# Performance work log

Measured on AMD Instinct MI355X. Metric: run time of the kernel, lower is better.

## Reference

```python
import jax, jax.numpy as jnp
import numpy as np

D = 16        # attention features
H = 8         # heads (head_dim = 2)
L = 8         # encoder layers
FF = 16       # dim_feedforward
K = 35        # conv kernel = stride
SEQ_IN = 3500 # input length -> 100 patches
EPS = 1e-5


def layer_norm(x, g, b):
    mu = jnp.mean(x, axis=-1, keepdims=True)
    var = jnp.mean((x - mu) ** 2, axis=-1, keepdims=True)
    return (x - mu) * jax.lax.rsqrt(var + EPS) * g + b


def setup_inputs() -> dict:
    key = jax.random.key(0)
    ks = jax.random.split(key, 24)
    B = 2048
    s = 0.1
    inp = {
        "x": jax.random.normal(ks[0], (B, SEQ_IN), dtype=jnp.float32),
        "conv_w": jax.random.normal(ks[1], (D, K), dtype=jnp.float32) * s,   # Conv1d(1->16,k=35)
        "conv_b": jax.random.normal(ks[2], (D,), dtype=jnp.float32) * s,
        "cls_emb": jax.random.normal(ks[3], (1, 1, D), dtype=jnp.float32),
        # stacked per-layer params [L, ...]
        "Wqkv": jax.random.normal(ks[4], (L, 3 * D, D), dtype=jnp.float32) * s,
        "bqkv": jnp.zeros((L, 3 * D), dtype=jnp.float32),
        "Wo": jax.random.normal(ks[5], (L, D, D), dtype=jnp.float32) * s,
        "bo": jnp.zeros((L, D), dtype=jnp.float32),
        "W1": jax.random.normal(ks[6], (L, FF, D), dtype=jnp.float32) * s,
        "b1": jnp.zeros((L, FF), dtype=jnp.float32),
        "W2": jax.random.normal(ks[7], (L, D, FF), dtype=jnp.float32) * s,
        "b2": jnp.zeros((L, D), dtype=jnp.float32),
        "ln1_g": jnp.ones((L, D), dtype=jnp.float32),
        "ln1_b": jnp.zeros((L, D), dtype=jnp.float32),
        "ln2_g": jnp.ones((L, D), dtype=jnp.float32),
        "ln2_b": jnp.zeros((L, D), dtype=jnp.float32),
        "lnf_g": jnp.ones((D,), dtype=jnp.float32),
        "lnf_b": jnp.zeros((D,), dtype=jnp.float32),
        "end_w": jax.random.normal(ks[8], (100, D), dtype=jnp.float32) * s,  # Conv1d(16->100,k=1)
        "end_b": jnp.zeros((100,), dtype=jnp.float32),
        "head_w": jax.random.normal(ks[9], (1, 100), dtype=jnp.float32) * s, # Linear(100->1)
        "head_b": jnp.zeros((1,), dtype=jnp.float32),
    }
    return inp


def _forward(x, conv_w, conv_b, cls_emb, Wqkv, bqkv, Wo, bo, W1, b1, W2, b2,
             ln1_g, ln1_b, ln2_g, ln2_b, lnf_g, lnf_b, end_w, end_b, head_w, head_b):
    B = x.shape[0]
    # patch embed: stride==kernel Conv1d == blocked matmul. [B,100,35] @ [35,16]
    patches = x.reshape(B, SEQ_IN // K, K)
    h = jnp.einsum("bpk,fk->bpf", patches, conv_w) + conv_b  # [B,100,16]
    h = jnp.concatenate([jnp.broadcast_to(cls_emb, (B, 1, D)), h], axis=1)  # [B,101,16]
    S = h.shape[1]
    scale = 1.0 / jnp.sqrt(jnp.asarray(D // H, dtype=h.dtype))

    def layer(hc, p):
        wqkv, bq, wo, bob, w1, b1l, w2, b2l, g1, be1, g2, be2 = p
        qkv = jnp.einsum("bsd,ed->bse", hc, wqkv) + bq      # [B,S,48]
        q, k, v = jnp.split(qkv, 3, axis=-1)
        q = q.reshape(B, S, H, D // H)
        k = k.reshape(B, S, H, D // H)
        v = v.reshape(B, S, H, D // H)
        scores = jnp.einsum("bshd,bthd->bhst", q, k) * scale  # [B,H,S,S]
        attn = jax.nn.softmax(scores, axis=-1)
        ctx = jnp.einsum("bhst,bthd->bshd", attn, v).reshape(B, S, D)
        attn_out = jnp.einsum("bsd,od->bso", ctx, wo) + bob
        hc = layer_norm(hc + attn_out, g1, be1)               # post-norm
        ff = jnp.einsum("bsd,fd->bsf", hc, w1) + b1l
        ff = jnp.einsum("bsf,df->bsd", jax.nn.relu(ff), w2) + b2l
        hc = layer_norm(hc + ff, g2, be2)
        return hc, None

    params = (Wqkv, bqkv, Wo, bo, W1, b1, W2, b2, ln1_g, ln1_b, ln2_g, ln2_b)
    h, _ = jax.lax.scan(layer, h, params)
    h = layer_norm(h, lnf_g, lnf_b)
    cls = h[:, 0, :]                                          # [B,16]
    latent = cls @ end_w.T + end_b                            # 1x1 conv == linear, [B,100]
    logits = latent @ head_w.T + head_b                       # [B,1]
    return jax.nn.sigmoid(logits)


def reference(x, conv_w, conv_b, cls_emb, Wqkv, bqkv, Wo, bo, W1, b1, W2, b2,
              ln1_g, ln1_b, ln2_g, ln2_b, lnf_g, lnf_b, end_w, end_b, head_w, head_b):
    return _forward(x, conv_w, conv_b, cls_emb, Wqkv, bqkv, Wo, bo, W1, b1, W2, b2,
                    ln1_g, ln1_b, ln2_g, ln2_b, lnf_g, lnf_b, end_w, end_b, head_w, head_b)
```

## Files before the change

kernel.cpp:

```cpp
#include <hip/hip_runtime.h>
#include <math.h>

#define DD   16
#define NH   8
#define NL   8
#define FFD  16
#define KK   35
#define SEQ  3500
#define NP   100
#define SS   101
#define NBATCH 2
#define NT   256
#define ROWDW 20
#define NROW 102
#define NWPAIR 6144

typedef __fp16 h2 __attribute__((ext_vector_type(2)));

__device__ __forceinline__ float fdot2(h2 a, h2 b, float c) {
#if __has_builtin(__builtin_amdgcn_fdot2)
  return __builtin_amdgcn_fdot2(a, b, c, false);
#else
  return c + (float)a.x * (float)b.x + (float)a.y * (float)b.y;
#endif
}
__device__ __forceinline__ float exp2_fast(float x) {
#if __has_builtin(__builtin_amdgcn_exp2f)
  return __builtin_amdgcn_exp2f(x);
#else
  return exp2f(x);
#endif
}
__device__ __forceinline__ float rcp_fast(float x) {
#if __has_builtin(__builtin_amdgcn_rcpf)
  return __builtin_amdgcn_rcpf(x);
#else
  return 1.0f / x;
#endif
}
__device__ __forceinline__ h2 pk_h2(float a, float b) {
#if __has_builtin(__builtin_amdgcn_cvt_pkrtz)
  return __builtin_amdgcn_cvt_pkrtz(a, b);
#else
  h2 r; r.x = (__fp16)a; r.y = (__fp16)b; return r;
#endif
}
__device__ __forceinline__ unsigned pk_u(float a, float b) {
  return __builtin_bit_cast(unsigned, pk_h2(a, b));
}
__device__ __forceinline__ h2 as_h2(unsigned u) {
  return __builtin_bit_cast(h2, u);
}

__device__ __forceinline__ void lnorm16(float* h, const float* __restrict__ g,
                                        const float* __restrict__ bb) {
  float mu = 0.f;
  #pragma unroll
  for (int d = 0; d < DD; ++d) mu += h[d];
  mu *= (1.f / DD);
  float var = 0.f;
  #pragma unroll
  for (int d = 0; d < DD; ++d) { float c = h[d] - mu; var += c * c; }
  var *= (1.f / DD);
  const float r = rsqrtf(var + 1e-5f);
  #pragma unroll
  for (int d = 0; d < DD; ++d) h[d] = (h[d] - mu) * r * g[d] + bb[d];
}

__device__ __forceinline__ float dot16(const h2* hv, const unsigned* __restrict__ w, float acc) {
  #pragma unroll
  for (int i = 0; i < 8; ++i) acc = fdot2(hv[i], as_h2(w[i]), acc);
  return acc;
}

__global__ __launch_bounds__(256)
void pack_weights(const float* __restrict__ Wqkv, const float* __restrict__ Wo,
                  const float* __restrict__ W1,   const float* __restrict__ W2,
                  unsigned* __restrict__ dst)
{
  const int i = blockIdx.x * 256 + threadIdx.x;
  if (i >= NWPAIR) return;
  float a, b;
  if (i < 3072)      { a = Wqkv[2*i];        b = Wqkv[2*i+1]; }
  else if (i < 4096) { int j = i - 3072; a = Wo[2*j]; b = Wo[2*j+1]; }
  else if (i < 5120) { int j = i - 4096; a = W1[2*j]; b = W1[2*j+1]; }
  else               { int j = i - 5120; a = W2[2*j]; b = W2[2*j+1]; }
  dst[i] = pk_u(a, b);
}

__global__ __launch_bounds__(NT, 4)
void transformer_fwd_g(const float* __restrict__ x,
                       const float* __restrict__ conv_w,  const float* __restrict__ conv_b,
                       const float* __restrict__ cls_emb,
                       const float* __restrict__ bqkv,
                       const float* __restrict__ bo,
                       const float* __restrict__ b1,
                       const float* __restrict__ b2,
                       const float* __restrict__ ln1_g,   const float* __restrict__ ln1_b,
                       const float* __restrict__ ln2_g,   const float* __restrict__ ln2_b,
                       const float* __restrict__ lnf_g,   const float* __restrict__ lnf_b,
                       const float* __restrict__ end_w,   const float* __restrict__ end_b,
                       const float* __restrict__ head_w,  const float* __restrict__ head_b,
                       float* __restrict__ out,
                       const unsigned* __restrict__ wpk, int B)
{
  __shared__ unsigned s_kv[NBATCH][NROW * ROWDW];
  __shared__ float s_cls[NBATCH][DD];
  __shared__ float s_lat[NBATCH][NP];

  const int tid  = threadIdx.x;
  const int wid  = tid >> 6;
  const int lane = tid & 63;
  const int j    = wid >> 1;
  const int r    = ((wid & 1) << 6) + lane;
  const int b    = blockIdx.x * NBATCH + j;
  const bool act = (r < SS) && (b < B);

  float h[DD];
  if (act) {
    if (r == 0) {
      #pragma unroll
      for (int d = 0; d < DD; ++d) h[d] = cls_emb[d];
    } else {
      const float* xp = x + (size_t)b * SEQ + (r - 1) * KK;
      float xv[KK];
      #pragma unroll
      for (int k = 0; k < KK; ++k) xv[k] = xp[k];
      #pragma unroll
      for (int f = 0; f < DD; ++f) {
        float acc = conv_b[f];
        #pragma unroll
        for (int k = 0; k < KK; ++k) acc += xv[k] * conv_w[f * KK + k];
        h[f] = acc;
      }
    }
  }

  const float qs = 1.4426950408889634f * 0.70710678118654752f;

  for (int l = 0; l < NL; ++l) {
    const unsigned* wq16 = wpk + l * 384;
    const unsigned* wo16 = wpk + 3072 + l * 128;
    const unsigned* w116 = wpk + 4096 + l * 128;
    const unsigned* w216 = wpk + 5120 + l * 128;
    const float* bq  = bqkv + l * (3 * DD);
    const float* bol = bo   + l * DD;
    const float* b1l = b1   + l * FFD;
    const float* b2l = b2   + l * DD;
    const float* g1  = ln1_g + l * DD;  const float* be1 = ln1_b + l * DD;
    const float* g2  = ln2_g + l * DD;  const float* be2 = ln2_b + l * DD;

    __syncthreads();

    h2 q2[NH];
    if (act) {
      h2 hv[8];
      #pragma unroll
      for (int i = 0; i < 8; ++i) hv[i] = pk_h2(h[2*i], h[2*i+1]);

      #pragma unroll
      for (int hh = 0; hh < NH; ++hh) {
        const float a0 = dot16(hv, &wq16[(2*hh    ) * 8], bq[2*hh]);
        const float a1 = dot16(hv, &wq16[(2*hh + 1) * 8], bq[2*hh+1]);
        q2[hh] = pk_h2(a0 * qs, a1 * qs);
      }
      unsigned row[16];
      #pragma unroll
      for (int e = 0; e < 16; e += 2) {
        const float a0 = dot16(hv, &wq16[(DD + e    ) * 8], bq[DD + e]);
        const float a1 = dot16(hv, &wq16[(DD + e + 1) * 8], bq[DD + e + 1]);
        row[e >> 1] = pk_u(a0, a1);
      }
      #pragma unroll
      for (int e = 0; e < 16; e += 2) {
        const float a0 = dot16(hv, &wq16[(2*DD + e    ) * 8], bq[2*DD + e]);
        const float a1 = dot16(hv, &wq16[(2*DD + e + 1) * 8], bq[2*DD + e + 1]);
        row[8 + (e >> 1)] = pk_u(a0, a1);
      }
      uint4* dst = (uint4*)&s_kv[j][r * ROWDW];
      dst[0] = make_uint4(row[0],  row[1],  row[2],  row[3]);
      dst[1] = make_uint4(row[4],  row[5],  row[6],  row[7]);
      dst[2] = make_uint4(row[8],  row[9],  row[10], row[11]);
      dst[3] = make_uint4(row[12], row[13], row[14], row[15]);
    }
    __syncthreads();

    if (act) {
      float lsum[NH], cxx[NH], cxy[NH];
      #pragma unroll
      for (int hh = 0; hh < NH; ++hh) { lsum[hh] = 0.f; cxx[hh] = 0.f; cxy[hh] = 0.f; }

      const uint4* kv = (const uint4*)&s_kv[j][0];
      uint4 c0 = kv[0], c1 = kv[1], c2 = kv[2], c3 = kv[3];
      #pragma unroll 2
      for (int t = 0; t < SS; ++t) {
        const uint4* np = kv + 5 * (t + 1);
        const uint4 n0 = np[0], n1 = np[1], n2 = np[2], n3 = np[3];

        const unsigned ku[8] = {c0.x, c0.y, c0.z, c0.w, c1.x, c1.y, c1.z, c1.w};
        const unsigned vu[8] = {c2.x, c2.y, c2.z, c2.w, c3.x, c3.y, c3.z, c3.w};
        #pragma unroll
        for (int hh = 0; hh < NH; ++hh) {
          const h2 kk = as_h2(ku[hh]);
          const h2 vv = as_h2(vu[hh]);
          const float p = exp2_fast(fdot2(q2[hh], kk, 0.0f));
          lsum[hh] += p;
          cxx[hh]  += (float)vv.x * p;
          cxy[hh]  += (float)vv.y * p;
        }
        c0 = n0; c1 = n1; c2 = n2; c3 = n3;
      }

      float cx[DD];
      #pragma unroll
      for (int hh = 0; hh < NH; ++hh) {
        const float inv = rcp_fast(lsum[hh]);
        cx[2 * hh]     = cxx[hh] * inv;
        cx[2 * hh + 1] = cxy[hh] * inv;
      }

      h2 cv[8];
      #pragma unroll
      for (int i = 0; i < 8; ++i) cv[i] = pk_h2(cx[2*i], cx[2*i+1]);
      #pragma unroll
      for (int od = 0; od < DD; ++od)
        h[od] += dot16(cv, &wo16[od * 8], bol[od]);
      lnorm16(h, g1, be1);

      h2 hv2[8];
      #pragma unroll
      for (int i = 0; i < 8; ++i) hv2[i] = pk_h2(h[2*i], h[2*i+1]);
      float fv[FFD];
      #pragma unroll
      for (int f = 0; f < FFD; ++f)
        fv[f] = fmaxf(dot16(hv2, &w116[f * 8], b1l[f]), 0.f);
      h2 fv2[8];
      #pragma unroll
      for (int i = 0; i < 8; ++i) fv2[i] = pk_h2(fv[2*i], fv[2*i+1]);
      #pragma unroll
      for (int od = 0; od < DD; ++od)
        h[od] += dot16(fv2, &w216[od * 8], b2l[od]);
      lnorm16(h, g2, be2);
    }
  }

  __syncthreads();
  if (act && r == 0) {
    lnorm16(h, lnf_g, lnf_b);
    #pragma unroll
    for (int d = 0; d < DD; ++d) s_cls[j][d] = h[d];
  }
  __syncthreads();
  if (tid < NBATCH * NP) {
    const int jj = tid / NP;
    const int oo = tid - jj * NP;
    if (blockIdx.x * NBATCH + jj < B) {
      float acc = end_b[oo];
      #pragma unroll
      for (int d = 0; d < DD; ++d) acc += s_cls[jj][d] * end_w[oo * DD + d];
      s_lat[jj][oo] = acc * head_w[oo];
    }
  }
  __syncthreads();
  if (tid < NBATCH) {
    const int bb = blockIdx.x * NBATCH + tid;
    if (bb < B) {
      float acc = head_b[0];
      for (int o = 0; o < NP; ++o) acc += s_lat[tid][o];
      out[bb] = rcp_fast(1.f + exp2_fast(-acc * 1.4426950408889634f));
    }
  }
}

#define FB_NBATCH 3
#define FB_NT 320
#define KROW 8
#define VROW 8
#define KREG (SS * KROW + 4)
#define VREG (SS * VROW + 2)
typedef float f2 __attribute__((ext_vector_type(2)));

__global__ __launch_bounds__(FB_NT)
void transformer_fwd_lds(const float* __restrict__ x,
                         const float* __restrict__ conv_w,  const float* __restrict__ conv_b,
                         const float* __restrict__ cls_emb,
                         const float* __restrict__ Wqkv,    const float* __restrict__ bqkv,
                         const float* __restrict__ Wo,      const float* __restrict__ bo,
                         const float* __restrict__ W1,      const float* __restrict__ b1,
                         const float* __restrict__ W2,      const float* __restrict__ b2,
                         const float* __restrict__ ln1_g,   const float* __restrict__ ln1_b,
                         const float* __restrict__ ln2_g,   const float* __restrict__ ln2_b,
                         const float* __restrict__ lnf_g,   const float* __restrict__ lnf_b,
                         const float* __restrict__ end_w,   const float* __restrict__ end_b,
                         const float* __restrict__ head_w,  const float* __restrict__ head_b,
                         float* __restrict__ out, int B)
{
  __shared__ h2    s_K[FB_NBATCH][KREG];
  __shared__ f2    s_V[FB_NBATCH][VREG];
  __shared__ float s_cls[FB_NBATCH][DD];
  __shared__ float s_lat[FB_NBATCH][NP];

  const int tid = threadIdx.x;
  const int j   = tid / SS;
  const int r   = tid - j * SS;
  const int b   = blockIdx.x * FB_NBATCH + j;
  const bool act = (tid < FB_NBATCH * SS) && (b < B);

  float h[DD];
  if (act) {
    if (r == 0) {
      #pragma unroll
      for (int d = 0; d < DD; ++d) h[d] = cls_emb[d];
    } else {
      const float* xp = x + (size_t)b * SEQ + (r - 1) * KK;
      float xv[KK];
      #pragma unroll
      for (int k = 0; k < KK; ++k) xv[k] = xp[k];
      #pragma unroll
      for (int f = 0; f < DD; ++f) {
        float acc = conv_b[f];
        #pragma unroll
        for (int k = 0; k < KK; ++k) acc += xv[k] * conv_w[f * KK + k];
        h[f] = acc;
      }
    }
  }

  const float qs = 1.4426950408889634f * 0.70710678118654752f;

  for (int l = 0; l < NL; ++l) {
    const float* wq  = Wqkv + l * (3 * DD * DD);
    const float* bq  = bqkv + l * (3 * DD);
    const float* wo  = Wo   + l * (DD * DD);
    const float* bol = bo   + l * DD;
    const float* w1  = W1   + l * (FFD * DD);
    const float* b1l = b1   + l * FFD;
    const float* w2  = W2   + l * (DD * FFD);
    const float* b2l = b2   + l * DD;
    const float* g1  = ln1_g + l * DD;  const float* be1 = ln1_b + l * DD;
    const float* g2  = ln2_g + l * DD;  const float* be2 = ln2_b + l * DD;

    __syncthreads();

    h2 q2[NH];
    if (act) {
      #pragma unroll
      for (int hh = 0; hh < NH; ++hh) {
        const int e0 = 2 * hh;
        float a0 = bq[e0], a1 = bq[e0 + 1];
        #pragma unroll
        for (int d = 0; d < DD; ++d) {
          a0 += h[d] * wq[e0 * DD + d];
          a1 += h[d] * wq[(e0 + 1) * DD + d];
        }
        q2[hh] = pk_h2(a0 * qs, a1 * qs);
      }
      h2* kw = &s_K[j][r * KROW];
      #pragma unroll
      for (int hh = 0; hh < NH; ++hh) {
        const int e0 = DD + 2 * hh;
        float a0 = bq[e0], a1 = bq[e0 + 1];
        #pragma unroll
        for (int d = 0; d < DD; ++d) {
          a0 += h[d] * wq[e0 * DD + d];
          a1 += h[d] * wq[(e0 + 1) * DD + d];
        }
        kw[hh] = pk_h2(a0, a1);
      }
      f2* vw = &s_V[j][r * VROW];
      #pragma unroll
      for (int hh = 0; hh < NH; ++hh) {
        const int e0 = 2 * DD + 2 * hh;
        float a0 = bq[e0], a1 = bq[e0 + 1];
        #pragma unroll
        for (int d = 0; d < DD; ++d) {
          a0 += h[d] * wq[e0 * DD + d];
          a1 += h[d] * wq[(e0 + 1) * DD + d];
        }
        f2 vv; vv.x = a0; vv.y = a1;
        vw[hh] = vv;
      }
    }
    __syncthreads();

    if (act) {
      float lsum[NH];
      f2 ctx[NH];
      #pragma unroll
      for (int hh = 0; hh < NH; ++hh) { lsum[hh] = 0.f; ctx[hh].x = 0.f; ctx[hh].y = 0.f; }
      const h2* kp0 = &s_K[j][0];
      const f2* vp0 = &s_V[j][0];
      for (int t = 0; t < SS; ++t) {
        const h2* kp = kp0 + t * KROW;
        const f2* vp = vp0 + t * VROW;
        #pragma unroll
        for (int hh = 0; hh < NH; ++hh) {
          const float p = exp2_fast(fdot2(q2[hh], kp[hh], 0.0f));
          lsum[hh] += p;
          ctx[hh]  += vp[hh] * p;
        }
      }
      float cx[DD];
      #pragma unroll
      for (int hh = 0; hh < NH; ++hh) {
        const float inv = rcp_fast(lsum[hh]);
        cx[2 * hh]     = ctx[hh].x * inv;
        cx[2 * hh + 1] = ctx[hh].y * inv;
      }
      #pragma unroll
      for (int od = 0; od < DD; ++od) {
        float acc = bol[od];
        #pragma unroll
        for (int d = 0; d < DD; ++d) acc += cx[d] * wo[od * DD + d];
        h[od] += acc;
      }
      lnorm16(h, g1, be1);
      float fv[FFD];
      #pragma unroll
      for (int f = 0; f < FFD; ++f) {
        float acc = b1l[f];
        #pragma unroll
        for (int d = 0; d < DD; ++d) acc += h[d] * w1[f * DD + d];
        fv[f] = fmaxf(acc, 0.f);
      }
      #pragma unroll
      for (int od = 0; od < DD; ++od) {
        float acc = b2l[od];
        #pragma unroll
        for (int f = 0; f < FFD; ++f) acc += fv[f] * w2[od * FFD + f];
        h[od] += acc;
      }
      lnorm16(h, g2, be2);
    }
  }

  __syncthreads();
  if (act && r == 0) {
    lnorm16(h, lnf_g, lnf_b);
    #pragma unroll
    for (int d = 0; d < DD; ++d) s_cls[j][d] = h[d];
  }
  __syncthreads();
  if (tid < FB_NBATCH * NP) {
    const int jj = tid / NP;
    const int oo = tid - jj * NP;
    if (blockIdx.x * FB_NBATCH + jj < B) {
      float acc = end_b[oo];
      #pragma unroll
      for (int d = 0; d < DD; ++d) acc += s_cls[jj][d] * end_w[oo * DD + d];
      s_lat[jj][oo] = acc * head_w[oo];
    }
  }
  __syncthreads();
  if (tid < FB_NBATCH) {
    const int bb = blockIdx.x * FB_NBATCH + tid;
    if (bb < B) {
      float acc = head_b[0];
      for (int o = 0; o < NP; ++o) acc += s_lat[tid][o];
      out[bb] = rcp_fast(1.f + exp2_fast(-acc * 1.4426950408889634f));
    }
  }
}

extern "C" void kernel_launch(void* const* d_in, const int* in_sizes, int n_in,
                              void* d_out, int out_size, void* d_ws, size_t ws_size,
                              hipStream_t stream) {
  const float* x       = (const float*)d_in[0];
  const float* conv_w  = (const float*)d_in[1];
  const float* conv_b  = (const float*)d_in[2];
  const float* cls_emb = (const float*)d_in[3];
  const float* Wqkv    = (const float*)d_in[4];
  const float* bqkv    = (const float*)d_in[5];
  const float* Wo      = (const float*)d_in[6];
  const float* bo      = (const float*)d_in[7];
  const float* W1      = (const float*)d_in[8];
  const float* b1      = (const float*)d_in[9];
  const float* W2      = (const float*)d_in[10];
  const float* b2      = (const float*)d_in[11];
  const float* ln1_g   = (const float*)d_in[12];
  const float* ln1_b   = (const float*)d_in[13];
  const float* ln2_g   = (const float*)d_in[14];
  const float* ln2_b   = (const float*)d_in[15];
  const float* lnf_g   = (const float*)d_in[16];
  const float* lnf_b   = (const float*)d_in[17];
  const float* end_w   = (const float*)d_in[18];
  const float* end_b   = (const float*)d_in[19];
  const float* head_w  = (const float*)d_in[20];
  const float* head_b  = (const float*)d_in[21];
  float* out = (float*)d_out;

  const int B = in_sizes[0] / SEQ;

  if (ws_size >= NWPAIR * sizeof(unsigned)) {
    unsigned* wpk = (unsigned*)d_ws;
    pack_weights<<<(NWPAIR + 255) / 256, 256, 0, stream>>>(Wqkv, Wo, W1, W2, wpk);
    const int nb = (B + NBATCH - 1) / NBATCH;
    transformer_fwd_g<<<nb, NT, 0, stream>>>(
        x, conv_w, conv_b, cls_emb, bqkv, bo, b1, b2,
        ln1_g, ln1_b, ln2_g, ln2_b, lnf_g, lnf_b, end_w, end_b, head_w, head_b,
        out, wpk, B);
  } else {
    const int nb = (B + FB_NBATCH - 1) / FB_NBATCH;
    transformer_fwd_lds<<<nb, FB_NT, 0, stream>>>(
        x, conv_w, conv_b, cls_emb, Wqkv, bqkv, Wo, bo, W1, b1, W2, b2,
        ln1_g, ln1_b, ln2_g, ln2_b, lnf_g, lnf_b, end_w, end_b, head_w, head_b,
        out, B);
  }
}
```

Measured before the change: 590.1 us.

## Stage K/V rows in global workspace and broadcast via scalar loads

Adds a new kernel that writes each layer's fp16 K/V rows to a global workspace instead of LDS. The attention loop reads them with s_load_dwordx16 into scalar registers, since every lane in a wave reads the same row. This aims to replace per-lane LDS broadcast reads with one scalar load per key. The risks are a serialized wait on each scalar load, global write-then-read coherence that relies on s_dcache_inv, and a larger workspace requirement. The old LDS fallback kernel is removed and the previous shared-memory kernel becomes the fallback.

```diff
diff --git a/kernel.cpp b/kernel.cpp
--- a/kernel.cpp
+++ b/kernel.cpp
@@ -11,11 +11,12 @@
 #define SS   101
 #define NBATCH 2
 #define NT   256
-#define ROWDW 20
-#define NROW 102
+#define ROWB 64
+#define BATB (SS * ROWB)
 #define NWPAIR 6144
 
 typedef __fp16 h2 __attribute__((ext_vector_type(2)));
+typedef int  v16i __attribute__((ext_vector_type(16)));
 
 __device__ __forceinline__ float fdot2(h2 a, h2 b, float c) {
 #if __has_builtin(__builtin_amdgcn_fdot2)
@@ -87,6 +88,195 @@
   else               { int j = i - 5120; a = W2[2*j]; b = W2[2*j+1]; }
   dst[i] = pk_u(a, b);
 }
+
+__global__ __launch_bounds__(NT, 4)
+void transformer_fwd_s(const float* __restrict__ x,
+                       const float* __restrict__ conv_w,  const float* __restrict__ conv_b,
+                       const float* __restrict__ cls_emb,
+                       const float* __restrict__ bqkv,
+                       const float* __restrict__ bo,
+                       const float* __restrict__ b1,
+                       const float* __restrict__ b2,
+                       const float* __restrict__ ln1_g,   const float* __restrict__ ln1_b,
+                       const float* __restrict__ ln2_g,   const float* __restrict__ ln2_b,
+                       const float* __restrict__ lnf_g,   const float* __restrict__ lnf_b,
+                       const float* __restrict__ end_w,   const float* __restrict__ end_b,
+                       const float* __restrict__ head_w,  const float* __restrict__ head_b,
+                       float* __restrict__ out, char* __restrict__ ws,
+                       const unsigned* __restrict__ wpk, int B)
+{
+  __shared__ float s_cls[NBATCH][DD];
+  __shared__ float s_lat[NBATCH][NP];
+
+  const int tid  = threadIdx.x;
+  const int wid  = tid >> 6;
+  const int lane = tid & 63;
+  const int j    = wid >> 1;
+  const int r    = ((wid & 1) << 6) + lane;
+  const int b    = blockIdx.x * NBATCH + j;
+  const bool act = (r < SS) && (b < B);
+
+  const int   b_u    = __builtin_amdgcn_readfirstlane(b);
+  const char* kvbase = ws + (size_t)b_u * BATB;
+  uint4*      kvw    = (uint4*)(ws + (size_t)b * BATB);
+
+  float h[DD];
+  #pragma unroll
+  for (int d = 0; d < DD; ++d) h[d] = 0.f;
+  if (act) {
+    if (r == 0) {
+      #pragma unroll
+      for (int d = 0; d < DD; ++d) h[d] = cls_emb[d];
+    } else {
+      const float* xp = x + (size_t)b * SEQ + (r - 1) * KK;
+      float xv[KK];
+      #pragma unroll
+      for (int k = 0; k < KK; ++k) xv[k] = xp[k];
+      #pragma unroll
+      for (int f = 0; f < DD; ++f) {
+        float acc = conv_b[f];
+        #pragma unroll
+        for (int k = 0; k < KK; ++k) acc += xv[k] * conv_w[f * KK + k];
+        h[f] = acc;
+      }
+    }
+  }
+
+  const float qs = 1.4426950408889634f * 0.70710678118654752f;
+
+  for (int l = 0; l < NL; ++l) {
+    const unsigned* wq16 = wpk + l * 384;
+    const unsigned* wo16 = wpk + 3072 + l * 128;
+    const unsigned* w116 = wpk + 4096 + l * 128;
+    const unsigned* w216 = wpk + 5120 + l * 128;
+    const float* bq  = bqkv + l * (3 * DD);
+    const float* bol = bo   + l * DD;
+    const float* b1l = b1   + l * FFD;
+    const float* b2l = b2   + l * DD;
+    const float* g1  = ln1_g + l * DD;  const float* be1 = ln1_b + l * DD;
+    const float* g2  = ln2_g + l * DD;  const float* be2 = ln2_b + l * DD;
+
+    __syncthreads();
+
+    h2 hv[8];
+    #pragma unroll
+    for (int i = 0; i < 8; ++i) hv[i] = pk_h2(h[2*i], h[2*i+1]);
+
+    h2 q2[NH];
+    #pragma unroll
+    for (int hh = 0; hh < NH; ++hh) {
+      const float a0 = dot16(hv, &wq16[(2*hh    ) * 8], bq[2*hh]);
+      const float a1 = dot16(hv, &wq16[(2*hh + 1) * 8], bq[2*hh+1]);
+      q2[hh] = pk_h2(a0 * qs, a1 * qs);
+    }
+    unsigned row[16];
+    #pragma unroll
+    for (int e = 0; e < 16; e += 2) {
+      const float a0 = dot16(hv, &wq16[(DD + e    ) * 8], bq[DD + e]);
+      const float a1 = dot16(hv, &wq16[(DD + e + 1) * 8], bq[DD + e + 1]);
+      row[e >> 1] = pk_u(a0, a1);
+    }
+    #pragma unroll
+    for (int e = 0; e < 16; e += 2) {
+      const float a0 = dot16(hv, &wq16[(2*DD + e    ) * 8], bq[2*DD + e]);
+      const float a1 = dot16(hv, &wq16[(2*DD + e + 1) * 8], bq[2*DD + e + 1]);
+      row[8 + (e >> 1)] = pk_u(a0, a1);
+    }
+    if (act) {
+      uint4* dst = kvw + (size_t)r * 4;
+      dst[0] = make_uint4(row[0],  row[1],  row[2],  row[3]);
+      dst[1] = make_uint4(row[4],  row[5],  row[6],  row[7]);
+      dst[2] = make_uint4(row[8],  row[9],  row[10], row[11]);
+      dst[3] = make_uint4(row[12], row[13], row[14], row[15]);
+    }
+    __syncthreads();
+
+    asm volatile("s_dcache_inv" ::: "memory");
+
+    float lsum[NH], cxx[NH], cxy[NH];
+    #pragma unroll
+    for (int hh = 0; hh < NH; ++hh) { lsum[hh] = 0.f; cxx[hh] = 0.f; cxy[hh] = 0.f; }
+
+    #pragma unroll 2
+    for (int t = 0; t < SS; ++t) {
+      v16i kv;
+      const char* ap = kvbase + (size_t)t * ROWB;
+      asm volatile("s_load_dwordx16 %0, %1, 0x0\n\t"
+                   "s_waitcnt lgkmcnt(0)"
+                   : "=s"(kv) : "s"(ap) : "memory");
+      #pragma unroll
+      for (int hh = 0; hh < NH; ++hh) {
+        const h2 kk = as_h2((unsigned)kv[hh]);
+        const h2 vv = as_h2((unsigned)kv[8 + hh]);
+        const float p = exp2_fast(fdot2(q2[hh], kk, 0.0f));
+        lsum[hh] += p;
+        cxx[hh]  += (float)vv.x * p;
+        cxy[hh]  += (float)vv.y * p;
+      }
+    }
+
+    float cx[DD];
+    #pragma unroll
+    for (int hh = 0; hh < NH; ++hh) {
+      const float inv = rcp_fast(lsum[hh]);
+      cx[2 * hh]     = cxx[hh] * inv;
+      cx[2 * hh + 1] = cxy[hh] * inv;
+    }
+
+    h2 cv[8];
+    #pragma unroll
+    for (int i = 0; i < 8; ++i) cv[i] = pk_h2(cx[2*i], cx[2*i+1]);
+    #pragma unroll
+    for (int od = 0; od < DD; ++od)
+      h[od] += dot16(cv, &wo16[od * 8], bol[od]);
+    lnorm16(h, g1, be1);
+
+    h2 hv2[8];
+    #pragma unroll
+    for (int i = 0; i < 8; ++i) hv2[i] = pk_h2(h[2*i], h[2*i+1]);
+    float fv[FFD];
+    #pragma unroll
+    for (int f = 0; f < FFD; ++f)
+      fv[f] = fmaxf(dot16(hv2, &w116[f * 8], b1l[f]), 0.f);
+    h2 fv2[8];
+    #pragma unroll
+    for (int i = 0; i < 8; ++i) fv2[i] = pk_h2(fv[2*i], fv[2*i+1]);
+    #pragma unroll
+    for (int od = 0; od < DD; ++od)
+      h[od] += dot16(fv2, &w216[od * 8], b2l[od]);
+    lnorm16(h, g2, be2);
+  }
+
+  __syncthreads();
+  if (act && r == 0) {
+    lnorm16(h, lnf_g, lnf_b);
+    #pragma unroll
+    for (int d = 0; d < DD; ++d) s_cls[j][d] = h[d];
+  }
+  __syncthreads();
+  if (tid < NBATCH * NP) {
+    const int jj = tid / NP;
+    const int oo = tid - jj * NP;
+    if (blockIdx.x * NBATCH + jj < B) {
+      float acc = end_b[oo];
+      #pragma unroll
+      for (int d = 0; d < DD; ++d) acc += s_cls[jj][d] * end_w[oo * DD + d];
+      s_lat[jj][oo] = acc * head_w[oo];
+    }
+  }
+  __syncthreads();
+  if (tid < NBATCH) {
+    const int bb = blockIdx.x * NBATCH + tid;
+    if (bb < B) {
+      float acc = head_b[0];
+      for (int o = 0; o < NP; ++o) acc += s_lat[tid][o];
+      out[bb] = rcp_fast(1.f + exp2_fast(-acc * 1.4426950408889634f));
+    }
+  }
+}
+
+#define ROWDW 20
+#define NROW 102
 
 __global__ __launch_bounds__(NT, 4)
 void transformer_fwd_g(const float* __restrict__ x,
@@ -157,7 +347,6 @@
       h2 hv[8];
       #pragma unroll
       for (int i = 0; i < 8; ++i) hv[i] = pk_h2(h[2*i], h[2*i+1]);
-
       #pragma unroll
       for (int hh = 0; hh < NH; ++hh) {
         const float a0 = dot16(hv, &wq16[(2*hh    ) * 8], bq[2*hh]);
@@ -189,14 +378,12 @@
       float lsum[NH], cxx[NH], cxy[NH];
       #pragma unroll
       for (int hh = 0; hh < NH; ++hh) { lsum[hh] = 0.f; cxx[hh] = 0.f; cxy[hh] = 0.f; }
-
       const uint4* kv = (const uint4*)&s_kv[j][0];
       uint4 c0 = kv[0], c1 = kv[1], c2 = kv[2], c3 = kv[3];
       #pragma unroll 2
       for (int t = 0; t < SS; ++t) {
         const uint4* np = kv + 5 * (t + 1);
         const uint4 n0 = np[0], n1 = np[1], n2 = np[2], n3 = np[3];
-
         const unsigned ku[8] = {c0.x, c0.y, c0.z, c0.w, c1.x, c1.y, c1.z, c1.w};
         const unsigned vu[8] = {c2.x, c2.y, c2.z, c2.w, c3.x, c3.y, c3.z, c3.w};
         #pragma unroll
@@ -210,7 +397,6 @@
         }
         c0 = n0; c1 = n1; c2 = n2; c3 = n3;
       }
-
       float cx[DD];
       #pragma unroll
       for (int hh = 0; hh < NH; ++hh) {
@@ -218,7 +404,6 @@
         cx[2 * hh]     = cxx[hh] * inv;
         cx[2 * hh + 1] = cxy[hh] * inv;
       }
-
       h2 cv[8];
       #pragma unroll
       for (int i = 0; i < 8; ++i) cv[i] = pk_h2(cx[2*i], cx[2*i+1]);
@@ -226,7 +411,6 @@
       for (int od = 0; od < DD; ++od)
         h[od] += dot16(cv, &wo16[od * 8], bol[od]);
       lnorm16(h, g1, be1);
-
       h2 hv2[8];
       #pragma unroll
       for (int i = 0; i < 8; ++i) hv2[i] = pk_h2(h[2*i], h[2*i+1]);
@@ -264,196 +448,6 @@
   __syncthreads();
   if (tid < NBATCH) {
     const int bb = blockIdx.x * NBATCH + tid;
-    if (bb < B) {
-      float acc = head_b[0];
-      for (int o = 0; o < NP; ++o) acc += s_lat[tid][o];
-      out[bb] = rcp_fast(1.f + exp2_fast(-acc * 1.4426950408889634f));
-    }
-  }
-}
-
-#define FB_NBATCH 3
-#define FB_NT 320
-#define KROW 8
-#define VROW 8
-#define KREG (SS * KROW + 4)
-#define VREG (SS * VROW + 2)
-typedef float f2 __attribute__((ext_vector_type(2)));
-
-__global__ __launch_bounds__(FB_NT)
-void transformer_fwd_lds(const float* __restrict__ x,
-                         const float* __restrict__ conv_w,  const float* __restrict__ conv_b,
-                         const float* __restrict__ cls_emb,
-                         const float* __restrict__ Wqkv,    const float* __restrict__ bqkv,
-                         const float* __restrict__ Wo,      const float* __restrict__ bo,
-                         const float* __restrict__ W1,      const float* __restrict__ b1,
-                         const float* __restrict__ W2,      const float* __restrict__ b2,
-                         const float* __restrict__ ln1_g,   const float* __restrict__ ln1_b,
-                         const float* __restrict__ ln2_g,   const float* __restrict__ ln2_b,
-                         const float* __restrict__ lnf_g,   const float* __restrict__ lnf_b,
-                         const float* __restrict__ end_w,   const float* __restrict__ end_b,
-                         const float* __restrict__ head_w,  const float* __restrict__ head_b,
-                         float* __restrict__ out, int B)
-{
-  __shared__ h2    s_K[FB_NBATCH][KREG];
-  __shared__ f2    s_V[FB_NBATCH][VREG];
-  __shared__ float s_cls[FB_NBATCH][DD];
-  __shared__ float s_lat[FB_NBATCH][NP];
-
-  const int tid = threadIdx.x;
-  const int j   = tid / SS;
-  const int r   = tid - j * SS;
-  const int b   = blockIdx.x * FB_NBATCH + j;
-  const bool act = (tid < FB_NBATCH * SS) && (b < B);
-
-  float h[DD];
-  if (act) {
-    if (r == 0) {
-      #pragma unroll
-      for (int d = 0; d < DD; ++d) h[d] = cls_emb[d];
-    } else {
-      const float* xp = x + (size_t)b * SEQ + (r - 1) * KK;
-      float xv[KK];
-      #pragma unroll
-      for (int k = 0; k < KK; ++k) xv[k] = xp[k];
-      #pragma unroll
-      for (int f = 0; f < DD; ++f) {
-        float acc = conv_b[f];
-        #pragma unroll
-        for (int k = 0; k < KK; ++k) acc += xv[k] * conv_w[f * KK + k];
-        h[f] = acc;
-      }
-    }
-  }
-
-  const float qs = 1.4426950408889634f * 0.70710678118654752f;
-
-  for (int l = 0; l < NL; ++l) {
-    const float* wq  = Wqkv + l * (3 * DD * DD);
-    const float* bq  = bqkv + l * (3 * DD);
-    const float* wo  = Wo   + l * (DD * DD);
-    const float* bol = bo   + l * DD;
-    const float* w1  = W1   + l * (FFD * DD);
-    const float* b1l = b1   + l * FFD;
-    const float* w2  = W2   + l * (DD * FFD);
-    const float* b2l = b2   + l * DD;
-    const float* g1  = ln1_g + l * DD;  const float* be1 = ln1_b + l * DD;
-    const float* g2  = ln2_g + l * DD;  const float* be2 = ln2_b + l * DD;
-
-    __syncthreads();
-
-    h2 q2[NH];
-    if (act) {
-      #pragma unroll
-      for (int hh = 0; hh < NH; ++hh) {
-        const int e0 = 2 * hh;
-        float a0 = bq[e0], a1 = bq[e0 + 1];
-        #pragma unroll
-        for (int d = 0; d < DD; ++d) {
-          a0 += h[d] * wq[e0 * DD + d];
-          a1 += h[d] * wq[(e0 + 1) * DD + d];
-        }
-        q2[hh] = pk_h2(a0 * qs, a1 * qs);
-      }
-      h2* kw = &s_K[j][r * KROW];
-      #pragma unroll
-      for (int hh = 0; hh < NH; ++hh) {
-        const int e0 = DD + 2 * hh;
-        float a0 = bq[e0], a1 = bq[e0 + 1];
-        #pragma unroll
-        for (int d = 0; d < DD; ++d) {
-          a0 += h[d] * wq[e0 * DD + d];
-          a1 += h[d] * wq[(e0 + 1) * DD + d];
-        }
-        kw[hh] = pk_h2(a0, a1);
-      }
-      f2* vw = &s_V[j][r * VROW];
-      #pragma unroll
-      for (int hh = 0; hh < NH; ++hh) {
-        const int e0 = 2 * DD + 2 * hh;
-        float a0 = bq[e0], a1 = bq[e0 + 1];
-        #pragma unroll
-        for (int d = 0; d < DD; ++d) {
-          a0 += h[d] * wq[e0 * DD + d];
-          a1 += h[d] * wq[(e0 + 1) * DD + d];
-        }
-        f2 vv; vv.x = a0; vv.y = a1;
-        vw[hh] = vv;
-      }
-    }
-    __syncthreads();
-
-    if (act) {
-      float lsum[NH];
-      f2 ctx[NH];
-      #pragma unroll
-      for (int hh = 0; hh < NH; ++hh) { lsum[hh] = 0.f; ctx[hh].x = 0.f; ctx[hh].y = 0.f; }
-      const h2* kp0 = &s_K[j][0];
-      const f2* vp0 = &s_V[j][0];
-      for (int t = 0; t < SS; ++t) {
-        const h2* kp = kp0 + t * KROW;
-        const f2* vp = vp0 + t * VROW;
-        #pragma unroll
-        for (int hh = 0; hh < NH; ++hh) {
-          const float p = exp2_fast(fdot2(q2[hh], kp[hh], 0.0f));
-          lsum[hh] += p;
-          ctx[hh]  += vp[hh] * p;
-        }
-      }
-      float cx[DD];
-      #pragma unroll
-      for (int hh = 0; hh < NH; ++hh) {
-        const float inv = rcp_fast(lsum[hh]);
-        cx[2 * hh]     = ctx[hh].x * inv;
-        cx[2 * hh + 1] = ctx[hh].y * inv;
-      }
-      #pragma unroll
-      for (int od = 0; od < DD; ++od) {
-        float acc = bol[od];
-        #pragma unroll
-        for (int d = 0; d < DD; ++d) acc += cx[d] * wo[od * DD + d];
-        h[od] += acc;
-      }
-      lnorm16(h, g1, be1);
-      float fv[FFD];
-      #pragma unroll
-      for (int f = 0; f < FFD; ++f) {
-        float acc = b1l[f];
-        #pragma unroll
-        for (int d = 0; d < DD; ++d) acc += h[d] * w1[f * DD + d];
-        fv[f] = fmaxf(acc, 0.f);
-      }
-      #pragma unroll
-      for (int od = 0; od < DD; ++od) {
-        float acc = b2l[od];
-        #pragma unroll
-        for (int f = 0; f < FFD; ++f) acc += fv[f] * w2[od * FFD + f];
-        h[od] += acc;
-      }
-      lnorm16(h, g2, be2);
-    }
-  }
-
-  __syncthreads();
-  if (act && r == 0) {
-    lnorm16(h, lnf_g, lnf_b);
-    #pragma unroll
-    for (int d = 0; d < DD; ++d) s_cls[j][d] = h[d];
-  }
-  __syncthreads();
-  if (tid < FB_NBATCH * NP) {
-    const int jj = tid / NP;
-    const int oo = tid - jj * NP;
-    if (blockIdx.x * FB_NBATCH + jj < B) {
-      float acc = end_b[oo];
-      #pragma unroll
-      for (int d = 0; d < DD; ++d) acc += s_cls[jj][d] * end_w[oo * DD + d];
-      s_lat[jj][oo] = acc * head_w[oo];
-    }
-  }
-  __syncthreads();
-  if (tid < FB_NBATCH) {
-    const int bb = blockIdx.x * FB_NBATCH + tid;
     if (bb < B) {
       float acc = head_b[0];
       for (int o = 0; o < NP; ++o) acc += s_lat[tid][o];
@@ -490,20 +484,22 @@
   float* out = (float*)d_out;
 
   const int B = in_sizes[0] / SEQ;
-
-  if (ws_size >= NWPAIR * sizeof(unsigned)) {
+  const size_t kv_bytes = (size_t)B * BATB;
+  const int nb = (B + NBATCH - 1) / NBATCH;
+
+  if (ws_size >= kv_bytes + NWPAIR * sizeof(unsigned)) {
+    unsigned* wpk = (unsigned*)((char*)d_ws + kv_bytes);
+    pack_weights<<<(NWPAIR + 255) / 256, 256, 0, stream>>>(Wqkv, Wo, W1, W2, wpk);
+    transformer_fwd_s<<<nb, NT, 0, stream>>>(
+        x, conv_w, conv_b, cls_emb, bqkv, bo, b1, b2,
+        ln1_g, ln1_b, ln2_g, ln2_b, lnf_g, lnf_b, end_w, end_b, head_w, head_b,
+        out, (char*)d_ws, wpk, B);
+  } else {
     unsigned* wpk = (unsigned*)d_ws;
     pack_weights<<<(NWPAIR + 255) / 256, 256, 0, stream>>>(Wqkv, Wo, W1, W2, wpk);
-    const int nb = (B + NBATCH - 1) / NBATCH;
     transformer_fwd_g<<<nb, NT, 0, stream>>>(
         x, conv_w, conv_b, cls_emb, bqkv, bo, b1, b2,
         ln1_g, ln1_b, ln2_g, ln2_b, lnf_g, lnf_b, end_w, end_b, head_w, head_b,
         out, wpk, B);
-  } else {
-    const int nb = (B + FB_NBATCH - 1) / FB_NBATCH;
-    transformer_fwd_lds<<<nb, FB_NT, 0, stream>>>(
-        x, conv_w, conv_b, cls_emb, Wqkv, bqkv, Wo, bo, W1, b1, W2, b2,
-        ln1_g, ln1_b, ln2_g, ln2_b, lnf_g, lnf_b, end_w, end_b, head_w, head_b,
-        out, B);
-  }
-}
+  }
+}
```

After: 646.7 us. 9.6% more time.

## Split attention key range across two wave pairs per sequence

Applied to the files above, without the earlier changes.

Each block now handles one sequence instead of two. The two wave pairs split the key/value range in half, each computing partial softmax sums, and exchange the partials through LDS as fp16. Only half the waves compute K/V and stash the residual in LDS, and the other half reload it after the merge. This halves the serial attention loop per thread and raises occupancy, at the cost of extra barriers, LDS traffic, duplicated Q and FFN work, and fp16 rounding of the partial sums. Because there is no max subtraction, the fp16 partials could overflow.

```diff
diff --git a/kernel.cpp b/kernel.cpp
--- a/kernel.cpp
+++ b/kernel.cpp
@@ -9,10 +9,14 @@
 #define SEQ  3500
 #define NP   100
 #define SS   101
-#define NBATCH 2
 #define NT   256
+#define TSPLIT 51
 #define ROWDW 20
-#define NROW 102
+#define PARTSTR 13
+#define KVDW  (SS * ROWDW)
+#define PARTDW (2 * SS * PARTSTR)
+#define UNIDW 2626
+#define HROW 17
 #define NWPAIR 6144
 
 typedef __fp16 h2 __attribute__((ext_vector_type(2)));
@@ -88,8 +92,8 @@
   dst[i] = pk_u(a, b);
 }
 
-__global__ __launch_bounds__(NT, 4)
-void transformer_fwd_g(const float* __restrict__ x,
+__global__ __launch_bounds__(NT, 8)
+void transformer_fwd_t(const float* __restrict__ x,
                        const float* __restrict__ conv_w,  const float* __restrict__ conv_b,
                        const float* __restrict__ cls_emb,
                        const float* __restrict__ bqkv,
@@ -102,19 +106,23 @@
                        const float* __restrict__ end_w,   const float* __restrict__ end_b,
                        const float* __restrict__ head_w,  const float* __restrict__ head_b,
                        float* __restrict__ out,
-                       const unsigned* __restrict__ wpk, int B)
+                       const unsigned* __restrict__ wpk)
 {
-  __shared__ unsigned s_kv[NBATCH][NROW * ROWDW];
-  __shared__ float s_cls[NBATCH][DD];
-  __shared__ float s_lat[NBATCH][NP];
-
-  const int tid  = threadIdx.x;
-  const int wid  = tid >> 6;
-  const int lane = tid & 63;
-  const int j    = wid >> 1;
-  const int r    = ((wid & 1) << 6) + lane;
-  const int b    = blockIdx.x * NBATCH + j;
-  const bool act = (r < SS) && (b < B);
+  __shared__ __align__(16) unsigned s_uni[UNIDW];
+  __shared__ float s_h[SS * HROW];
+  __shared__ float s_cls[DD];
+  __shared__ float s_lat[NP];
+
+  const int tid   = threadIdx.x;
+  const int wid   = tid >> 6;
+  const int lane  = tid & 63;
+  const int qhalf = wid & 1;
+  const int khalf = wid >> 1;
+  const int r     = (qhalf << 6) + lane;
+  const bool act  = (r < SS);
+  const int tA    = khalf ? TSPLIT : 0;
+  const int tB    = khalf ? SS : TSPLIT;
+  const size_t b  = blockIdx.x;
 
   float h[DD];
   if (act) {
@@ -122,7 +130,7 @@
       #pragma unroll
       for (int d = 0; d < DD; ++d) h[d] = cls_emb[d];
     } else {
-      const float* xp = x + (size_t)b * SEQ + (r - 1) * KK;
+      const float* xp = x + b * SEQ + (r - 1) * KK;
       float xv[KK];
       #pragma unroll
       for (int k = 0; k < KK; ++k) xv[k] = xp[k];
@@ -154,6 +162,10 @@
 
     h2 q2[NH];
     if (act) {
+      if (khalf == 0) {
+        #pragma unroll
+        for (int d = 0; d < DD; ++d) s_h[r * HROW + d] = h[d];
+      }
       h2 hv[8];
       #pragma unroll
       for (int i = 0; i < 8; ++i) hv[i] = pk_h2(h[2*i], h[2*i+1]);
@@ -164,41 +176,40 @@
         const float a1 = dot16(hv, &wq16[(2*hh + 1) * 8], bq[2*hh+1]);
         q2[hh] = pk_h2(a0 * qs, a1 * qs);
       }
-      unsigned row[16];
-      #pragma unroll
-      for (int e = 0; e < 16; e += 2) {
-        const float a0 = dot16(hv, &wq16[(DD + e    ) * 8], bq[DD + e]);
-        const float a1 = dot16(hv, &wq16[(DD + e + 1) * 8], bq[DD + e + 1]);
-        row[e >> 1] = pk_u(a0, a1);
-      }
-      #pragma unroll
-      for (int e = 0; e < 16; e += 2) {
-        const float a0 = dot16(hv, &wq16[(2*DD + e    ) * 8], bq[2*DD + e]);
-        const float a1 = dot16(hv, &wq16[(2*DD + e + 1) * 8], bq[2*DD + e + 1]);
-        row[8 + (e >> 1)] = pk_u(a0, a1);
-      }
-      uint4* dst = (uint4*)&s_kv[j][r * ROWDW];
-      dst[0] = make_uint4(row[0],  row[1],  row[2],  row[3]);
-      dst[1] = make_uint4(row[4],  row[5],  row[6],  row[7]);
-      dst[2] = make_uint4(row[8],  row[9],  row[10], row[11]);
-      dst[3] = make_uint4(row[12], row[13], row[14], row[15]);
+      if (khalf == 0) {
+        unsigned row[16];
+        #pragma unroll
+        for (int e = 0; e < 16; e += 2) {
+          const float a0 = dot16(hv, &wq16[(DD + e    ) * 8], bq[DD + e]);
+          const float a1 = dot16(hv, &wq16[(DD + e + 1) * 8], bq[DD + e + 1]);
+          row[e >> 1] = pk_u(a0, a1);
+        }
+        #pragma unroll
+        for (int e = 0; e < 16; e += 2) {
+          const float a0 = dot16(hv, &wq16[(2*DD + e    ) * 8], bq[2*DD + e]);
+          const float a1 = dot16(hv, &wq16[(2*DD + e + 1) * 8], bq[2*DD + e + 1]);
+          row[8 + (e >> 1)] = pk_u(a0, a1);
+        }
+        uint4* dst = (uint4*)&s_uni[r * ROWDW];
+        dst[0] = make_uint4(row[0],  row[1],  row[2],  row[3]);
+        dst[1] = make_uint4(row[4],  row[5],  row[6],  row[7]);
+        dst[2] = make_uint4(row[8],  row[9],  row[10], row[11]);
+        dst[3] = make_uint4(row[12], row[13], row[14], row[15]);
+      }
     }
     __syncthreads();
 
+    float lsum[NH], cxx[NH], cxy[NH];
+    #pragma unroll
+    for (int hh = 0; hh < NH; ++hh) { lsum[hh] = 0.f; cxx[hh] = 0.f; cxy[hh] = 0.f; }
+
     if (act) {
-      float lsum[NH], cxx[NH], cxy[NH];
-      #pragma unroll
-      for (int hh = 0; hh < NH; ++hh) { lsum[hh] = 0.f; cxx[hh] = 0.f; cxy[hh] = 0.f; }
-
-      const uint4* kv = (const uint4*)&s_kv[j][0];
-      uint4 c0 = kv[0], c1 = kv[1], c2 = kv[2], c3 = kv[3];
+      const uint4* kvu = (const uint4*)s_uni;
       #pragma unroll 2
-      for (int t = 0; t < SS; ++t) {
-        const uint4* np = kv + 5 * (t + 1);
-        const uint4 n0 = np[0], n1 = np[1], n2 = np[2], n3 = np[3];
-
-        const unsigned ku[8] = {c0.x, c0.y, c0.z, c0.w, c1.x, c1.y, c1.z, c1.w};
-        const unsigned vu[8] = {c2.x, c2.y, c2.z, c2.w, c3.x, c3.y, c3.z, c3.w};
+      for (int t = tA; t < tB; ++t) {
+        const uint4 a0 = kvu[5*t+0], a1 = kvu[5*t+1], a2 = kvu[5*t+2], a3 = kvu[5*t+3];
+        const unsigned ku[8] = {a0.x, a0.y, a0.z, a0.w, a1.x, a1.y, a1.z, a1.w};
+        const unsigned vu[8] = {a2.x, a2.y, a2.z, a2.w, a3.x, a3.y, a3.z, a3.w};
         #pragma unroll
         for (int hh = 0; hh < NH; ++hh) {
           const h2 kk = as_h2(ku[hh]);
@@ -208,7 +219,37 @@
           cxx[hh]  += (float)vv.x * p;
           cxy[hh]  += (float)vv.y * p;
         }
-        c0 = n0; c1 = n1; c2 = n2; c3 = n3;
+      }
+    }
+    __syncthreads();
+
+    if (act) {
+      unsigned* pp = &s_uni[(khalf * SS + r) * PARTSTR];
+      #pragma unroll
+      for (int i = 0; i < 4; ++i) pp[i]     = pk_u(lsum[2*i], lsum[2*i+1]);
+      #pragma unroll
+      for (int i = 0; i < 4; ++i) pp[4 + i] = pk_u(cxx[2*i],  cxx[2*i+1]);
+      #pragma unroll
+      for (int i = 0; i < 4; ++i) pp[8 + i] = pk_u(cxy[2*i],  cxy[2*i+1]);
+    }
+    __syncthreads();
+
+    if (act) {
+      const unsigned* qq = &s_uni[((1 - khalf) * SS + r) * PARTSTR];
+      #pragma unroll
+      for (int i = 0; i < 4; ++i) {
+        const h2 o = as_h2(qq[i]);
+        lsum[2*i] += (float)o.x;  lsum[2*i+1] += (float)o.y;
+      }
+      #pragma unroll
+      for (int i = 0; i < 4; ++i) {
+        const h2 o = as_h2(qq[4 + i]);
+        cxx[2*i] += (float)o.x;  cxx[2*i+1] += (float)o.y;
+      }
+      #pragma unroll
+      for (int i = 0; i < 4; ++i) {
+        const h2 o = as_h2(qq[8 + i]);
+        cxy[2*i] += (float)o.x;  cxy[2*i+1] += (float)o.y;
       }
 
       float cx[DD];
@@ -219,6 +260,8 @@
         cx[2 * hh + 1] = cxy[hh] * inv;
       }
 
+      #pragma unroll
+      for (int d = 0; d < DD; ++d) h[d] = s_h[r * HROW + d];
       h2 cv[8];
       #pragma unroll
       for (int i = 0; i < 8; ++i) cv[i] = pk_h2(cx[2*i], cx[2*i+1]);
@@ -245,30 +288,23 @@
   }
 
   __syncthreads();
-  if (act && r == 0) {
+  if (act && r == 0 && khalf == 0) {
     lnorm16(h, lnf_g, lnf_b);
     #pragma unroll
-    for (int d = 0; d < DD; ++d) s_cls[j][d] = h[d];
+    for (int d = 0; d < DD; ++d) s_cls[d] = h[d];
   }
   __syncthreads();
-  if (tid < NBATCH * NP) {
-    const int jj = tid / NP;
-    const int oo = tid - jj * NP;
-    if (blockIdx.x * NBATCH + jj < B) {
-      float acc = end_b[oo];
-      #pragma unroll
-      for (int d = 0; d < DD; ++d) acc += s_cls[jj][d] * end_w[oo * DD + d];
-      s_lat[jj][oo] = acc * head_w[oo];
-    }
+  if (tid < NP) {
+    float acc = end_b[tid];
+    #pragma unroll
+    for (int d = 0; d < DD; ++d) acc += s_cls[d] * end_w[tid * DD + d];
+    s_lat[tid] = acc * head_w[tid];
   }
   __syncthreads();
-  if (tid < NBATCH) {
-    const int bb = blockIdx.x * NBATCH + tid;
-    if (bb < B) {
-      float acc = head_b[0];
-      for (int o = 0; o < NP; ++o) acc += s_lat[tid][o];
-      out[bb] = rcp_fast(1.f + exp2_fast(-acc * 1.4426950408889634f));
-    }
+  if (tid == 0) {
+    float acc = head_b[0];
+    for (int o = 0; o < NP; ++o) acc += s_lat[o];
+    out[b] = rcp_fast(1.f + exp2_fast(-acc * 1.4426950408889634f));
   }
 }
 
@@ -494,11 +530,10 @@
   if (ws_size >= NWPAIR * sizeof(unsigned)) {
     unsigned* wpk = (unsigned*)d_ws;
     pack_weights<<<(NWPAIR + 255) / 256, 256, 0, stream>>>(Wqkv, Wo, W1, W2, wpk);
-    const int nb = (B + NBATCH - 1) / NBATCH;
-    transformer_fwd_g<<<nb, NT, 0, stream>>>(
+    transformer_fwd_t<<<B, NT, 0, stream>>>(
         x, conv_w, conv_b, cls_emb, bqkv, bo, b1, b2,
         ln1_g, ln1_b, ln2_g, ln2_b, lnf_g, lnf_b, end_w, end_b, head_w, head_b,
-        out, wpk, B);
+        out, wpk);
   } else {
     const int nb = (B + FB_NBATCH - 1) / FB_NBATCH;
     transformer_fwd_lds<<<nb, FB_NT, 0, stream>>>(
```

After: 764.7 us. 29.6% more time.
